# Performance work log

Hardware: AMD Instinct MI355X
Metric: run time of the kernel (lower is better)

Reference implementation:

```python
import jax, jax.numpy as jnp
import numpy as np

BATCH_SIZE = 4096
D = 128
TEMPERATURE = 0.5
EPS = 1e-8  # torch CosineSimilarity eps


def _neg_indices(batch_size):
    # flat indices of the (N, N-2) negative entries: all but diagonal and the +/-B pair
    N = 2 * batch_size
    mask = np.ones((N, N), dtype=bool)
    np.fill_diagonal(mask, False)
    i = np.arange(batch_size)
    mask[i, batch_size + i] = False
    mask[batch_size + i, i] = False
    return np.where(mask.ravel())[0]


NEG_IDX = jnp.asarray(_neg_indices(BATCH_SIZE))


def setup_inputs() -> dict:
    key = jax.random.key(0)
    k1, k2 = jax.random.split(key)
    return {
        "z_i": jax.random.normal(k1, (BATCH_SIZE, D), dtype=jnp.float32),
        "z_j": jax.random.normal(k2, (BATCH_SIZE, D), dtype=jnp.float32),
    }


def reference(z_i, z_j):
    batch_size = z_i.shape[0]
    N = 2 * batch_size
    z = jnp.concatenate([z_i, z_j], axis=0)                       # [N, D]
    norm = jnp.maximum(jnp.linalg.norm(z, axis=1, keepdims=True), EPS)
    zn = z / norm
    sim = (zn @ zn.T) / TEMPERATURE                               # [N, N] cosine sim / temp
    # positives: diagonals at offset +/- batch_size
    pos = jnp.concatenate(
        [jnp.diagonal(sim, offset=batch_size), jnp.diagonal(sim, offset=-batch_size)],
        axis=0,
    )                                                             # [N]
    neg = sim.ravel()[NEG_IDX].reshape(N, N - 2)                  # masked gather
    logits = jnp.concatenate([pos[:, None], neg], axis=1)         # [N, N-1], label = 0
    # CrossEntropyLoss(reduction='sum') with labels all 0, then / N
    loss = jnp.sum(jax.nn.logsumexp(logits, axis=1) - logits[:, 0]) / N
    return loss
```

## Files before the change

kernel.cpp:

```cpp
#include <hip/hip_runtime.h>
#include <hip/hip_bf16.h>


#define BATCH 4096
#define N_TOT 8192
#define DIM 128
#define ROWS_PER_WAVE 32
#define WAVES_PER_BLK 8
#define ROWS_PER_BLK 256
#define NROWBLK (N_TOT / ROWS_PER_BLK)
#define TILE_C 64

#define C_LOG2E2 2.8853900817779268f

using bf16x8 = __attribute__((ext_vector_type(8))) __bf16;
using f32x4  = __attribute__((ext_vector_type(4))) float;

typedef __attribute__((address_space(1))) const void cg_void;
typedef __attribute__((address_space(3))) void lds_void;
__device__ __forceinline__ void gll16(const void* g, void* l) {
    __builtin_amdgcn_global_load_lds((cg_void*)g, (lds_void*)l, 16, 0, 0);
}

__global__ __launch_bounds__(256) void k_normalize(const float* __restrict__ zi,
                                                   const float* __restrict__ zj,
                                                   __hip_bfloat16* __restrict__ zn) {
    int row  = blockIdx.x * 4 + (threadIdx.x >> 6);
    int lane = threadIdx.x & 63;
    const float* src = (row < BATCH) ? (zi + (size_t)row * DIM)
                                     : (zj + (size_t)(row - BATCH) * DIM);
    float2 v = ((const float2*)src)[lane];
    float ss = v.x * v.x + v.y * v.y;
    #pragma unroll
    for (int m = 1; m < 64; m <<= 1) ss += __shfl_xor(ss, m);
    float inv = 1.0f / fmaxf(sqrtf(ss), 1e-8f);
    __hip_bfloat162 o;
    o.x = __float2bfloat16(v.x * inv);
    o.y = __float2bfloat16(v.y * inv);
    ((__hip_bfloat162*)(zn + (size_t)row * DIM))[lane] = o;
}

template <int NCS>
__global__ __launch_bounds__(512, 4) void k_main(const __hip_bfloat16* __restrict__ zn_,
                                                 float* __restrict__ S_part) {
    constexpr int STRIP = N_TOT / NCS;
    constexpr int NT    = STRIP / TILE_C;

    __shared__ __align__(16) char Bs[2][TILE_C * 256];

    const int tid  = threadIdx.x;
    const int lane = tid & 63;
    const int wv   = tid >> 6;
    const int l15  = lane & 15;
    const int lb   = lane >> 4;
    const int wr0  = blockIdx.x * ROWS_PER_BLK + wv * ROWS_PER_WAVE;
    const int cs0  = blockIdx.y * STRIP;

    const __bf16* zn = (const __bf16*)zn_;

    bf16x8 a_[2][4];
    #pragma unroll
    for (int g = 0; g < 2; ++g) {
        const __bf16* p = zn + (size_t)(wr0 + g * 16 + l15) * DIM + lb * 8;
        #pragma unroll
        for (int s = 0; s < 4; ++s)
            a_[g][s] = *(const bf16x8*)(p + s * 32);
    }

    const char* gB = (const char*)(zn + (size_t)cs0 * DIM);
    int srcoff[2];
    #pragma unroll
    for (int i = 0; i < 2; ++i) {
        int m = i * 512 + tid;
        int c = m >> 4, slot = m & 15;
        int j = slot ^ (c & 7);
        srcoff[i] = c * 256 + j * 16;
    }

    auto STAGE = [&](int t) {
        const char* src = gB + (size_t)t * (TILE_C * 256);
        char* dst = Bs[t & 1];
        #pragma unroll
        for (int i = 0; i < 2; ++i)
            gll16(src + srcoff[i], dst + i * 8192 + wv * 1024);
    };

    f32x4 sumexp[2] = {};

    auto COMPUTE = [&](int t) {
        const char* buf = Bs[t & 1];
        const int c0t = cs0 + t * TILE_C;
        const bool diagtile = ((unsigned)(wr0 - c0t) < (unsigned)TILE_C);
        #pragma unroll
        for (int cb = 0; cb < 4; ++cb) {
            const int c = cb * 16 + l15;
            const char* pc = buf + c * 256;
            bf16x8 b[4];
            #pragma unroll
            for (int s = 0; s < 4; ++s)
                b[s] = *(const bf16x8*)(pc + ((lb + s * 4) ^ (c & 7)) * 16);
            f32x4 acc[2] = {};
            #pragma unroll
            for (int g = 0; g < 2; ++g)
                #pragma unroll
                for (int s = 0; s < 4; ++s)
                    acc[g] = __builtin_amdgcn_mfma_f32_16x16x32_bf16(a_[g][s], b[s], acc[g], 0, 0, 0);
            const int mycol = c0t + c;
            if (diagtile) {
                #pragma unroll
                for (int g = 0; g < 2; ++g)
                    #pragma unroll
                    for (int v = 0; v < 4; ++v) {
                        float e = __builtin_amdgcn_exp2f(acc[g][v] * C_LOG2E2);
                        int row = wr0 + g * 16 + lb * 4 + v;
                        sumexp[g][v] += (mycol == row) ? 0.0f : e;
                    }
            } else {
                #pragma unroll
                for (int g = 0; g < 2; ++g)
                    #pragma unroll
                    for (int v = 0; v < 4; ++v)
                        sumexp[g][v] += __builtin_amdgcn_exp2f(acc[g][v] * C_LOG2E2);
            }
        }
    };

    STAGE(0);
    __syncthreads();
    for (int t = 0; t < NT; ++t) {
        if (t + 1 < NT) STAGE(t + 1);
        COMPUTE(t);
        if (t + 1 < NT) __syncthreads();
    }

    #pragma unroll
    for (int m = 1; m <= 8; m <<= 1)
        #pragma unroll
        for (int g = 0; g < 2; ++g)
            #pragma unroll
            for (int v = 0; v < 4; ++v)
                sumexp[g][v] += __shfl_xor(sumexp[g][v], m);

    if (l15 == 0) {
        #pragma unroll
        for (int g = 0; g < 2; ++g) {
            int row = wr0 + g * 16 + lb * 4;
            *(f32x4*)&S_part[(size_t)blockIdx.y * N_TOT + row] = sumexp[g];
        }
    }
}

__device__ inline float bdot(unsigned a, unsigned b) {
    float alo = __uint_as_float(a << 16), ahi = __uint_as_float(a & 0xffff0000u);
    float blo = __uint_as_float(b << 16), bhi = __uint_as_float(b & 0xffff0000u);
    return fmaf(alo, blo, ahi * bhi);
}

template <int NSPLIT>
__global__ __launch_bounds__(256) void k_rowsum(const float* __restrict__ S_part,
                                                const __hip_bfloat16* __restrict__ zn_,
                                                float* __restrict__ blk_out) {
    const int r = blockIdx.x * 256 + threadIdx.x;
    float S = 0.0f;
    #pragma unroll
    for (int s = 0; s < NSPLIT; ++s) S += S_part[(size_t)s * N_TOT + r];

    const uint4* pa = (const uint4*)((const __bf16*)zn_ + (size_t)r * DIM);
    const uint4* pb = (const uint4*)((const __bf16*)zn_ + (size_t)(r ^ BATCH) * DIM);
    float dot = 0.0f;
    #pragma unroll
    for (int c = 0; c < DIM / 8; ++c) {
        uint4 ua = pa[c], ub = pb[c];
        dot += bdot(ua.x, ub.x) + bdot(ua.y, ub.y) + bdot(ua.z, ub.z) + bdot(ua.w, ub.w);
    }

    float contrib = __logf(S) - 2.0f * dot;

    #pragma unroll
    for (int m = 1; m < 64; m <<= 1) contrib += __shfl_xor(contrib, m);
    __shared__ float sm[4];
    if ((threadIdx.x & 63) == 0) sm[threadIdx.x >> 6] = contrib;
    __syncthreads();
    if (threadIdx.x == 0) blk_out[blockIdx.x] = sm[0] + sm[1] + sm[2] + sm[3];
}

__global__ void k_final(const float* __restrict__ blk_out, float* __restrict__ out) {
    float v = (threadIdx.x < NROWBLK) ? blk_out[threadIdx.x] : 0.0f;
    #pragma unroll
    for (int m = 1; m < 64; m <<= 1) v += __shfl_xor(v, m);
    if (threadIdx.x == 0) out[0] = v / (float)N_TOT;
}

extern "C" void kernel_launch(void* const* d_in, const int* in_sizes, int n_in,
                              void* d_out, int out_size, void* d_ws, size_t ws_size,
                              hipStream_t stream) {
    const float* zi = (const float*)d_in[0];
    const float* zj = (const float*)d_in[1];
    char* ws = (char*)d_ws;
    __hip_bfloat16* zn = (__hip_bfloat16*)ws;
    float* S_part = (float*)(ws + (size_t)2 * 1024 * 1024);
    float* out    = (float*)d_out;

    constexpr int NS = 16;
    float* blk = (float*)(ws + (size_t)2 * 1024 * 1024 + (size_t)NS * N_TOT * 4);

    k_normalize<<<N_TOT / 4, 256, 0, stream>>>(zi, zj, zn);
    k_main<NS><<<dim3(NROWBLK, NS), 512, 0, stream>>>(zn, S_part);
    k_rowsum<NS><<<NROWBLK, 256, 0, stream>>>(S_part, zn, blk);
    k_final<<<1, 64, 0, stream>>>(blk, out);
}
```

Measured before the change: 36.62 us.

## Exploit similarity matrix symmetry by computing only upper-triangular block pairs

The main kernel now iterates over the upper-triangular set of 256x256 block pairs (I<=J) instead of the full 8192x8192 grid. Each off-diagonal tile contributes row sums to rows of I and column sums, accumulated in shared memory across waves, to rows of J. This roughly halves the MFMA and exp work. In exchange it adds shuffles and LDS accumulation per column block, a serial loop to decode the pair index, and a grid of 528 blocks that may balance less evenly. k_rowsum now sums 32 partial contributions instead of 16.

```diff
diff --git a/kernel.cpp b/kernel.cpp
--- a/kernel.cpp
+++ b/kernel.cpp
@@ -8,8 +8,10 @@
 #define ROWS_PER_WAVE 32
 #define WAVES_PER_BLK 8
 #define ROWS_PER_BLK 256
-#define NROWBLK (N_TOT / ROWS_PER_BLK)
+#define NGRP 32
+#define NPAIR ((NGRP * (NGRP + 1)) / 2)
 #define TILE_C 64
+#define NT 4
 
 #define C_LOG2E2 2.8853900817779268f
 
@@ -40,21 +42,24 @@
     ((__hip_bfloat162*)(zn + (size_t)row * DIM))[lane] = o;
 }
 
-template <int NCS>
 __global__ __launch_bounds__(512, 4) void k_main(const __hip_bfloat16* __restrict__ zn_,
-                                                 float* __restrict__ S_part) {
-    constexpr int STRIP = N_TOT / NCS;
-    constexpr int NT    = STRIP / TILE_C;
-
+                                                 float* __restrict__ S_contrib) {
     __shared__ __align__(16) char Bs[2][TILE_C * 256];
+    __shared__ float colred[WAVES_PER_BLK][ROWS_PER_BLK];
 
     const int tid  = threadIdx.x;
     const int lane = tid & 63;
     const int wv   = tid >> 6;
     const int l15  = lane & 15;
     const int lb   = lane >> 4;
-    const int wr0  = blockIdx.x * ROWS_PER_BLK + wv * ROWS_PER_WAVE;
-    const int cs0  = blockIdx.y * STRIP;
+
+    int I = 0, rem = blockIdx.x;
+    while (rem >= NGRP - I) { rem -= NGRP - I; ++I; }
+    const int J = I + rem;
+    const bool isdiag = (I == J);
+
+    const int wr0 = I * ROWS_PER_BLK + wv * ROWS_PER_WAVE;
+    const int cs0 = J * ROWS_PER_BLK;
 
     const __bf16* zn = (const __bf16*)zn_;
 
@@ -66,6 +71,8 @@
         for (int s = 0; s < 4; ++s)
             a_[g][s] = *(const bf16x8*)(p + s * 32);
     }
+
+    ((float4*)colred)[tid] = float4{0.f, 0.f, 0.f, 0.f};
 
     const char* gB = (const char*)(zn + (size_t)cs0 * DIM);
     int srcoff[2];
@@ -116,17 +123,28 @@
                         sumexp[g][v] += (mycol == row) ? 0.0f : e;
                     }
             } else {
+                float cs = 0.0f;
                 #pragma unroll
                 for (int g = 0; g < 2; ++g)
                     #pragma unroll
-                    for (int v = 0; v < 4; ++v)
-                        sumexp[g][v] += __builtin_amdgcn_exp2f(acc[g][v] * C_LOG2E2);
+                    for (int v = 0; v < 4; ++v) {
+                        float e = __builtin_amdgcn_exp2f(acc[g][v] * C_LOG2E2);
+                        sumexp[g][v] += e;
+                        cs += e;
+                    }
+                if (!isdiag) {
+                    cs += __shfl_xor(cs, 16);
+                    cs += __shfl_xor(cs, 32);
+                    if (lb == 0)
+                        colred[wv][t * TILE_C + cb * 16 + l15] += cs;
+                }
             }
         }
     };
 
     STAGE(0);
     __syncthreads();
+    #pragma unroll
     for (int t = 0; t < NT; ++t) {
         if (t + 1 < NT) STAGE(t + 1);
         COMPUTE(t);
@@ -145,7 +163,17 @@
         #pragma unroll
         for (int g = 0; g < 2; ++g) {
             int row = wr0 + g * 16 + lb * 4;
-            *(f32x4*)&S_part[(size_t)blockIdx.y * N_TOT + row] = sumexp[g];
+            *(f32x4*)&S_contrib[(size_t)J * N_TOT + row] = sumexp[g];
+        }
+    }
+
+    if (!isdiag) {
+        __syncthreads();
+        if (tid < ROWS_PER_BLK) {
+            float s = 0.0f;
+            #pragma unroll
+            for (int w = 0; w < WAVES_PER_BLK; ++w) s += colred[w][tid];
+            S_contrib[(size_t)I * N_TOT + cs0 + tid] = s;
         }
     }
 }
@@ -156,14 +184,13 @@
     return fmaf(alo, blo, ahi * bhi);
 }
 
-template <int NSPLIT>
-__global__ __launch_bounds__(256) void k_rowsum(const float* __restrict__ S_part,
+__global__ __launch_bounds__(256) void k_rowsum(const float* __restrict__ S_contrib,
                                                 const __hip_bfloat16* __restrict__ zn_,
                                                 float* __restrict__ blk_out) {
     const int r = blockIdx.x * 256 + threadIdx.x;
     float S = 0.0f;
     #pragma unroll
-    for (int s = 0; s < NSPLIT; ++s) S += S_part[(size_t)s * N_TOT + r];
+    for (int s = 0; s < NGRP; ++s) S += S_contrib[(size_t)s * N_TOT + r];
 
     const uint4* pa = (const uint4*)((const __bf16*)zn_ + (size_t)r * DIM);
     const uint4* pb = (const uint4*)((const __bf16*)zn_ + (size_t)(r ^ BATCH) * DIM);
@@ -185,7 +212,7 @@
 }
 
 __global__ void k_final(const float* __restrict__ blk_out, float* __restrict__ out) {
-    float v = (threadIdx.x < NROWBLK) ? blk_out[threadIdx.x] : 0.0f;
+    float v = (threadIdx.x < NGRP) ? blk_out[threadIdx.x] : 0.0f;
     #pragma unroll
     for (int m = 1; m < 64; m <<= 1) v += __shfl_xor(v, m);
     if (threadIdx.x == 0) out[0] = v / (float)N_TOT;
@@ -198,14 +225,12 @@
     const float* zj = (const float*)d_in[1];
     char* ws = (char*)d_ws;
     __hip_bfloat16* zn = (__hip_bfloat16*)ws;
-    float* S_part = (float*)(ws + (size_t)2 * 1024 * 1024);
-    float* out    = (float*)d_out;
-
-    constexpr int NS = 16;
-    float* blk = (float*)(ws + (size_t)2 * 1024 * 1024 + (size_t)NS * N_TOT * 4);
+    float* S_contrib = (float*)(ws + (size_t)2 * 1024 * 1024);
+    float* blk       = (float*)(ws + (size_t)3 * 1024 * 1024);
+    float* out       = (float*)d_out;
 
     k_normalize<<<N_TOT / 4, 256, 0, stream>>>(zi, zj, zn);
-    k_main<NS><<<dim3(NROWBLK, NS), 512, 0, stream>>>(zn, S_part);
-    k_rowsum<NS><<<NROWBLK, 256, 0, stream>>>(S_part, zn, blk);
+    k_main<<<NPAIR, 512, 0, stream>>>(zn, S_contrib);
+    k_rowsum<<<NGRP, 256, 0, stream>>>(S_contrib, zn, blk);
     k_final<<<1, 64, 0, stream>>>(blk, out);
 }
```

New measurement: 44.16 us. 1.21x slower.
